# Optimization experiments

Measured on AMD Instinct MI355X. Metric: run time of the kernel, lower is better.

## Reference

```python
import math
import jax, jax.numpy as jnp
import numpy as np


def setup_inputs() -> dict:
    key = jax.random.key(0)
    ks = jax.random.split(key, 11)
    B, L, D = 16, 2048, 1024
    s = 0.02  # weight init scale
    return {
        "queries": jax.random.normal(ks[0], (B, L, D), jnp.float32),
        "keys": jax.random.normal(ks[1], (B, L, D), jnp.float32),
        "values": jax.random.normal(ks[2], (B, L, D), jnp.float32),
        "Wq": jax.random.normal(ks[3], (D, D), jnp.float32) * s,
        "bq": jax.random.normal(ks[4], (D,), jnp.float32) * s,
        "Wk": jax.random.normal(ks[5], (D, D), jnp.float32) * s,
        "bk": jax.random.normal(ks[6], (D,), jnp.float32) * s,
        "Wv": jax.random.normal(ks[7], (D, D), jnp.float32) * s,
        "bv": jax.random.normal(ks[8], (D,), jnp.float32) * s,
        "Wo": jax.random.normal(ks[9], (D, D), jnp.float32) * s,
        "bo": jax.random.normal(ks[10], (D,), jnp.float32) * s,
        "n_heads": 8,
    }


def reference(queries, keys, values, Wq, bq, Wk, bk, Wv, bv, Wo, bo, n_heads):
    B, L, D = queries.shape
    H = n_heads
    E = D // H
    # projections -> (B, H, E, L)
    q = (queries @ Wq.T + bq).reshape(B, L, H, E).transpose(0, 2, 3, 1)
    k = (keys @ Wk.T + bk).reshape(B, L, H, E).transpose(0, 2, 3, 1)
    v = (values @ Wv.T + bv).reshape(B, L, H, E).transpose(0, 2, 3, 1)

    # period-based dependency discovery via FFT cross-correlation
    q_fft = jnp.fft.rfft(q, axis=-1)
    k_fft = jnp.fft.rfft(k, axis=-1)
    corr = jnp.fft.irfft(q_fft * jnp.conj(k_fft), n=L, axis=-1)  # (B,H,E,L)

    # time-delay aggregation (training variant: batch-shared top-k delays)
    top_k = int(1 * math.log(L))  # factor = 1
    mean_value = corr.mean(axis=(1, 2))  # (B, L)
    _, index = jax.lax.top_k(mean_value.mean(axis=0), top_k)  # (top_k,)
    weights = mean_value[:, index]  # (B, top_k)
    tmp_corr = jax.nn.softmax(weights, axis=-1)  # (B, top_k)

    pos = jnp.arange(L)
    agg = jnp.zeros_like(v)
    for i in range(top_k):  # small fixed loop (top_k = 7)
        rolled = jnp.take(v, (pos + index[i]) % L, axis=-1)  # roll(v, -index[i])
        agg = agg + rolled * tmp_corr[:, i][:, None, None, None]

    out = agg.transpose(0, 3, 1, 2).reshape(B, L, D)  # (B,L,H,E) -> (B,L,D)
    return out @ Wo.T + bo
```

## Files before the change

### kernel.cpp

```cpp
#include <hip/hip_runtime.h>

typedef __attribute__((ext_vector_type(8))) short bf16x8;
typedef __attribute__((ext_vector_type(4))) short s16x4;
typedef __attribute__((ext_vector_type(4))) float f32x4;
typedef unsigned short ushort_t;

__device__ __forceinline__ float bf2f(unsigned short u) {
    union { unsigned int u; float f; } x; x.u = ((unsigned int)u) << 16; return x.f;
}
__device__ __forceinline__ unsigned short f2bf(float f) {
    union { float f; unsigned int u; } x; x.f = f;
    unsigned int u = x.u;
    unsigned int r = (u + 0x7fffu + ((u >> 16) & 1u)) >> 16;
    return (unsigned short)r;
}

#define GLDS16(gp, lp)                                                        \
    __builtin_amdgcn_global_load_lds(                                         \
        (const __attribute__((address_space(1))) void*)(gp),                  \
        (__attribute__((address_space(3))) void*)(lp), 16, 0, 0)

template<int OUT_MODE>
__device__ __forceinline__
void gemm_body(const unsigned short* __restrict__ A, const unsigned short* __restrict__ Bw,
               const float* __restrict__ bias, void* __restrict__ out_,
               int bid, int nb, unsigned short* sAp, unsigned short* sBp) {
    const int tid  = threadIdx.x;
    const int lane = tid & 63;
    const int w    = tid >> 6;
    const int wr   = w >> 2, wc = w & 3;
    const int fr   = lane & 15, g4 = lane >> 4;

    const int qq  = nb >> 3;
    const int swz = qq ? (bid & 7) * qq + (bid >> 3) : bid;
    const int  col0 = (swz & 3) * 256;
    const long row0 = (long)(swz >> 2) * 256;

    const int srow = tid >> 3;
    const int sj   = (tid & 7) ^ (srow & 7);
    const unsigned short* gA = A  + (size_t)(row0 + srow) * 1024 + sj * 8;
    const unsigned short* gB = Bw + (size_t)(col0 + srow) * 1024 + sj * 8;
    const int ldst = w * 1024;

    auto stage = [&](int buf, int t) {
        const unsigned short* a = gA + t * 64;
        const unsigned short* b = gB + t * 64;
        char* dA = (char*)(sAp + buf * 16384);
        char* dB = (char*)(sBp + buf * 16384);
#pragma unroll
        for (int r = 0; r < 4; ++r)
            GLDS16(a + r * 65536, (__attribute__((address_space(3))) char*)(dA + r * 8192 + ldst));
#pragma unroll
        for (int r = 0; r < 4; ++r)
            GLDS16(b + r * 65536, (__attribute__((address_space(3))) char*)(dB + r * 8192 + ldst));
    };

    f32x4 acc[8][4];
#pragma unroll
    for (int m = 0; m < 8; ++m)
#pragma unroll
        for (int n = 0; n < 4; ++n) acc[m][n] = (f32x4){0.f, 0.f, 0.f, 0.f};

    stage(0, 0);
    stage(1, 1);

    const int mskK = (fr & 7) << 4;

    for (int t = 0; t < 16; ++t) {
        if (t < 15) asm volatile("s_waitcnt vmcnt(8)" ::: "memory");
        else        asm volatile("s_waitcnt vmcnt(0)" ::: "memory");
        asm volatile("s_barrier" ::: "memory");
        __builtin_amdgcn_sched_barrier(0);

        const char* la = (const char*)(sAp + (t & 1) * 16384);
        const char* lb = (const char*)(sBp + (t & 1) * 16384);

        bf16x8 bF[2][4];
#pragma unroll
        for (int c = 0; c < 2; ++c)
#pragma unroll
            for (int n = 0; n < 4; ++n) {
                const int row = wc * 64 + n * 16 + fr;
                bF[c][n] = *(const bf16x8*)(lb + row * 128 + ((c * 64 + g4 * 16) ^ mskK));
            }
#pragma unroll
        for (int mh = 0; mh < 2; ++mh) {
            bf16x8 aF[2][4];
#pragma unroll
            for (int c = 0; c < 2; ++c)
#pragma unroll
                for (int m = 0; m < 4; ++m) {
                    const int row = wr * 128 + mh * 64 + m * 16 + fr;
                    aF[c][m] = *(const bf16x8*)(la + row * 128 + ((c * 64 + g4 * 16) ^ mskK));
                }
            __builtin_amdgcn_s_setprio(1);
#pragma unroll
            for (int c = 0; c < 2; ++c)
#pragma unroll
                for (int n = 0; n < 4; ++n)
#pragma unroll
                    for (int m = 0; m < 4; ++m)
                        acc[mh * 4 + m][n] =
                            __builtin_amdgcn_mfma_f32_16x16x32_bf16(aF[c][m], bF[c][n], acc[mh * 4 + m][n], 0, 0, 0);
            __builtin_amdgcn_s_setprio(0);
        }

        __builtin_amdgcn_sched_barrier(0);
        asm volatile("s_barrier" ::: "memory");
        if (t + 2 < 16) stage(t & 1, t + 2);
    }

    const int cr = g4 * 4;
    const int cc = fr;
    if constexpr (OUT_MODE == 2) {
        const int b  = (int)(row0 >> 11);
        const int tb = ((int)row0 & 2047) + wr * 128 + cr;
#pragma unroll
        for (int m = 0; m < 8; ++m) {
#pragma unroll
            for (int n = 0; n < 4; ++n) {
                int col = col0 + wc * 64 + n * 16 + cc;
                float bv = bias[col];
                s16x4 o;
#pragma unroll
                for (int j = 0; j < 4; ++j) o[j] = (short)f2bf(acc[m][n][j] + bv);
                *(s16x4*)&((unsigned short*)out_)[((size_t)b * 1024 + col) * 2048 + tb + m * 16] = o;
            }
        }
    } else {
#pragma unroll
        for (int m = 0; m < 8; ++m) {
            long row = row0 + wr * 128 + m * 16 + cr;
#pragma unroll
            for (int n = 0; n < 4; ++n) {
                int col = col0 + wc * 64 + n * 16 + cc;
                float bv = bias[col];
#pragma unroll
                for (int j = 0; j < 4; ++j) {
                    float v = acc[m][n][j] + bv;
                    if constexpr (OUT_MODE == 1) ((float*)out_)[(row + j) * 1024 + col] = v;
                    else ((unsigned short*)out_)[(row + j) * 1024 + col] = f2bf(v);
                }
            }
        }
    }
}

template<int OUT_MODE>
__global__ __launch_bounds__(512, 2)
void gemm256(const unsigned short* __restrict__ A, const unsigned short* __restrict__ Bw,
             const float* __restrict__ bias, void* __restrict__ out_) {
    __shared__ __align__(16) unsigned short sA[2][16384];
    __shared__ __align__(16) unsigned short sB[2][16384];
    gemm_body<OUT_MODE>(A, Bw, bias, out_, blockIdx.x, gridDim.x, &sA[0][0], &sB[0][0]);
}

__global__ __launch_bounds__(512, 2)
void gemm_pair(const unsigned short* __restrict__ A0, const unsigned short* __restrict__ B0,
               const float* __restrict__ bias0, void* __restrict__ o0,
               const unsigned short* __restrict__ A1, const unsigned short* __restrict__ B1,
               const float* __restrict__ bias1, void* __restrict__ o1) {
    __shared__ __align__(16) unsigned short sA[2][16384];
    __shared__ __align__(16) unsigned short sB[2][16384];
    if (blockIdx.x < 16)
        gemm_body<0>(A0, B0, bias0, o0, blockIdx.x, 16, &sA[0][0], &sB[0][0]);
    else
        gemm_body<0>(A1, B1, bias1, o1, blockIdx.x - 16, 16, &sA[0][0], &sB[0][0]);
}

__global__ __launch_bounds__(256)
void cast_f2b(const float* __restrict__ src, unsigned short* __restrict__ dst) {
    const size_t i = ((size_t)blockIdx.x * 256 + threadIdx.x) * 8;
    f32x4 v0 = *(const f32x4*)(src + i);
    f32x4 v1 = *(const f32x4*)(src + i + 4);
    bf16x8 o;
#pragma unroll
    for (int j = 0; j < 4; ++j) o[j] = (short)f2bf(v0[j]);
#pragma unroll
    for (int j = 0; j < 4; ++j) o[4 + j] = (short)f2bf(v1[j]);
    *(bf16x8*)(dst + i) = o;
}

__global__ __launch_bounds__(256)
void prep_all(const float* __restrict__ Wq, const float* __restrict__ Wk,
              const float* __restrict__ Wv, const float* __restrict__ Wo,
              const float* __restrict__ bv, const float* __restrict__ bo,
              unsigned short* __restrict__ wo, unsigned short* __restrict__ wvT,
              unsigned short* __restrict__ wqT, unsigned short* __restrict__ wkT,
              float* __restrict__ G, float* __restrict__ zb, float* __restrict__ b2) {
    __shared__ float tsm[64][65];
    const int bx  = blockIdx.x;
    const int tid = threadIdx.x;

    if (bx < 768) {
        const float* src = (bx < 256) ? Wv : (bx < 512) ? Wq : Wk;
        unsigned short* dst = (bx < 256) ? wvT : (bx < 512) ? wqT : wkT;
        const int t  = bx & 255;
        const int b0 = (t & 15) * 64;
        const int by = (t >> 4) * 64;
        const int tx = tid & 63, ty = tid >> 6;
        for (int r = ty; r < 64; r += 4)
            tsm[r][tx] = src[(size_t)(by + r) * 1024 + b0 + tx];
        __syncthreads();
        for (int r = ty; r < 64; r += 4)
            dst[(size_t)(b0 + r) * 1024 + by + tx] = f2bf(tsm[tx][r]);
    } else if (bx < 1024) {
        const int base = (bx - 768) * 4096 + tid * 4;
#pragma unroll
        for (int r = 0; r < 4; ++r) {
            const int i = base + r * 1024;
            f32x4 v = *(const f32x4*)(Wo + i);
            s16x4 o;
#pragma unroll
            for (int j = 0; j < 4; ++j) o[j] = (short)f2bf(v[j]);
            *(s16x4*)(wo + i) = o;
        }
    } else if (bx < 1033) {
        const int base = (bx - 1024) * 4096;
#pragma unroll
        for (int r = 0; r < 16; ++r) {
            const int i = base + r * 256 + tid;
            if (i < 32800) G[i] = 0.0f;
        }
    } else if (bx == 1033) {
        *(f32x4*)(zb + tid * 4) = (f32x4){0.f, 0.f, 0.f, 0.f};
    } else {
        const int n = (bx - 1034) * 4 + (tid >> 6);
        const int lane = tid & 63;
        float s = 0.f;
        for (int k = lane; k < 1024; k += 64) s += Wo[(size_t)n * 1024 + k] * bv[k];
#pragma unroll
        for (int off = 32; off > 0; off >>= 1) s += __shfl_xor(s, off, 64);
        if (lane == 0) b2[n] = s + bo[n];
    }
}

__device__ __forceinline__ void dft8(float* xr, float* xi) {
    const float c8 = 0.70710678118654752440f;
    float es0r = xr[0] + xr[4], es0i = xi[0] + xi[4];
    float es1r = xr[0] - xr[4], es1i = xi[0] - xi[4];
    float es2r = xr[2] + xr[6], es2i = xi[2] + xi[6];
    float es3r = xr[2] - xr[6], es3i = xi[2] - xi[6];
    float E0r = es0r + es2r, E0i = es0i + es2i;
    float E2r = es0r - es2r, E2i = es0i - es2i;
    float E1r = es1r + es3i, E1i = es1i - es3r;
    float E3r = es1r - es3i, E3i = es1i + es3r;
    float os0r = xr[1] + xr[5], os0i = xi[1] + xi[5];
    float os1r = xr[1] - xr[5], os1i = xi[1] - xi[5];
    float os2r = xr[3] + xr[7], os2i = xi[3] + xi[7];
    float os3r = xr[3] - xr[7], os3i = xi[3] - xi[7];
    float O0r = os0r + os2r, O0i = os0i + os2i;
    float O2r = os0r - os2r, O2i = os0i - os2i;
    float O1r = os1r + os3i, O1i = os1i - os3r;
    float O3r = os1r - os3i, O3i = os1i + os3r;
    float p1 = c8 * (O1r + O1i), q1 = c8 * (O1i - O1r);
    float p3 = c8 * (O3r + O3i), q3 = c8 * (O3i - O3r);
    xr[0] = E0r + O0r; xi[0] = E0i + O0i;
    xr[4] = E0r - O0r; xi[4] = E0i - O0i;
    xr[1] = E1r + p1;  xi[1] = E1i + q1;
    xr[5] = E1r - p1;  xi[5] = E1i - q1;
    xr[2] = E2r + O2i; xi[2] = E2i - O2r;
    xr[6] = E2r - O2i; xi[6] = E2i + O2r;
    xr[3] = E3r + q3;  xi[3] = E3i - p3;
    xr[7] = E3r - q3;  xi[7] = E3i + p3;
}

__device__ __forceinline__ int ps(int p) { return p ^ (((p >> 5) & 7) << 2); }

#define TWIDDLE2(wr_, wi_)                                                    \
    {                                                                         \
        float cr_ = (wr_), ci_ = (wi_);                                       \
        _Pragma("unroll")                                                     \
        for (int k = 1; k < 8; ++k) {                                         \
            float t0 = ar[k] * cr_ - ai[k] * ci_;                             \
            float t1 = ar[k] * ci_ + ai[k] * cr_;                             \
            ar[k] = t0; ai[k] = t1;                                           \
            float t2 = br[k] * cr_ - bi[k] * ci_;                             \
            float t3 = br[k] * ci_ + bi[k] * cr_;                             \
            br[k] = t2; bi[k] = t3;                                           \
            if (k < 7) {                                                      \
                float nr = cr_ * (wr_) - ci_ * (wi_);                         \
                float ni = cr_ * (wi_) + ci_ * (wr_);                         \
                cr_ = nr; ci_ = ni;                                           \
            }                                                                 \
        }                                                                     \
    }

__global__ __launch_bounds__(256)
void fft_corr(const float* __restrict__ qf, const unsigned short* __restrict__ kt,
              float* __restrict__ G) {
    __shared__ float2 za[2048];
    __shared__ float2 zb[2048];
    const int tid = threadIdx.x;
    const int bid = blockIdx.x;
    const int swzb = (bid & 7) * 256 + (bid >> 3);
    const int b = swzb >> 7;
    const int chunk = swzb & 127;

    const float N2PI = -6.28318530717958647692f;
    float w1r, w1i, w2r, w2i, w3r, w3i;
    {
        float s, c;
        __sincosf(N2PI * (float)tid * (1.0f / 2048.0f), &s, &c); w1r = c; w1i = s;
        __sincosf(N2PI * (float)(tid & 31) * (1.0f / 256.0f), &s, &c); w2r = c; w2i = s;
        __sincosf(N2PI * (float)(tid & 3) * (1.0f / 32.0f),  &s, &c); w3r = c; w3i = s;
    }

    f32x4 qreg0[8], qreg1[8];
    {
        const float* qb0 = qf + (size_t)b * 2048 * 1024 + chunk * 8;
#pragma unroll
        for (int k = 0; k < 8; ++k) {
            const float* p = qb0 + (size_t)(tid + 256 * k) * 1024;
            qreg0[k] = *(const f32x4*)p;
            qreg1[k] = *(const f32x4*)(p + 4);
        }
    }

    float aR0 = 0.f, aI0 = 0.f, aR1 = 0.f, aI1 = 0.f;
    float aR2 = 0.f, aI2 = 0.f, aR3 = 0.f, aI3 = 0.f, aR4 = 0.f;

    const int beta = tid >> 5, s2 = tid & 31;
    const int gam  = tid >> 2, u3 = tid & 3;

    for (int it = 0; it < 4; ++it) {
        const int d0 = chunk * 8 + it * 2;
        const unsigned short* k0 = kt + ((size_t)b * 1024 + d0) * 2048;
        const unsigned short* k1 = k0 + 2048;

        float ar[8], ai[8], br[8], bi[8];
#pragma unroll
        for (int k = 0; k < 8; ++k) {
            const int t = tid + 256 * k;
            f32x4 v = (it & 2) ? qreg1[k] : qreg0[k];
            float qa = (it & 1) ? v[2] : v[0];
            float qb = (it & 1) ? v[3] : v[1];
            ar[k] = qa; br[k] = qb;
            ai[k] = bf2f(k0[t]); bi[k] = bf2f(k1[t]);
        }
        dft8(ar, ai); dft8(br, bi);
        TWIDDLE2(w1r, w1i)
#pragma unroll
        for (int k = 0; k < 8; ++k) {
            const int p = ps(256 * k + tid);
            za[p] = make_float2(ar[k], ai[k]);
            zb[p] = make_float2(br[k], bi[k]);
        }
        __syncthreads();

#pragma unroll
        for (int k = 0; k < 8; ++k) {
            const int p = ps(256 * beta + 32 * k + s2);
            float2 va = za[p]; ar[k] = va.x; ai[k] = va.y;
            float2 vb = zb[p]; br[k] = vb.x; bi[k] = vb.y;
        }
        dft8(ar, ai); dft8(br, bi);
        TWIDDLE2(w2r, w2i)
#pragma unroll
        for (int k = 0; k < 8; ++k) {
            const int p = ps(256 * beta + 32 * k + s2);
            za[p] = make_float2(ar[k], ai[k]);
            zb[p] = make_float2(br[k], bi[k]);
        }
        __syncthreads();

#pragma unroll
        for (int k = 0; k < 8; ++k) {
            const int p = ps(32 * gam + 4 * k + u3);
            float2 va = za[p]; ar[k] = va.x; ai[k] = va.y;
            float2 vb = zb[p]; br[k] = vb.x; bi[k] = vb.y;
        }
        dft8(ar, ai); dft8(br, bi);
        TWIDDLE2(w3r, w3i)
#pragma unroll
        for (int k = 0; k < 8; ++k) {
            const int p = ps(32 * gam + 4 * k + u3);
            za[p] = make_float2(ar[k], ai[k]);
            zb[p] = make_float2(br[k], bi[k]);
        }
        __syncthreads();

#pragma unroll
        for (int k = 0; k < 8; ++k) {
            const int p = ps(8 * tid + k);
            float2 va = za[p]; ar[k] = va.x; ai[k] = va.y;
            float2 vb = zb[p]; br[k] = vb.x; bi[k] = vb.y;
        }
        __syncthreads();

#pragma unroll
        for (int blk = 0; blk < 2; ++blk) {
            const int o = 4 * blk;
            {
                float s0r = ar[o] + ar[o + 2], s0i = ai[o] + ai[o + 2];
                float s1r = ar[o] - ar[o + 2], s1i = ai[o] - ai[o + 2];
                float s2r = ar[o + 1] + ar[o + 3], s2i = ai[o + 1] + ai[o + 3];
                float s3r = ar[o + 1] - ar[o + 3], s3i = ai[o + 1] - ai[o + 3];
                ar[o + 0] = s0r + s2r; ai[o + 0] = s0i + s2i;
                ar[o + 2] = s0r - s2r; ai[o + 2] = s0i - s2i;
                ar[o + 1] = s1r + s3i; ai[o + 1] = s1i - s3r;
                ar[o + 3] = s1r - s3i; ai[o + 3] = s1i + s3r;
            }
            {
                float s0r = br[o] + br[o + 2], s0i = bi[o] + bi[o + 2];
                float s1r = br[o] - br[o + 2], s1i = bi[o] - bi[o + 2];
                float s2r = br[o + 1] + br[o + 3], s2i = bi[o + 1] + bi[o + 3];
                float s3r = br[o + 1] - br[o + 3], s3i = bi[o + 1] - bi[o + 3];
                br[o + 0] = s0r + s2r; bi[o + 0] = s0i + s2i;
                br[o + 2] = s0r - s2r; bi[o + 2] = s0i - s2i;
                br[o + 1] = s1r + s3i; bi[o + 1] = s1i - s3r;
                br[o + 3] = s1r - s3i; bi[o + 3] = s1i + s3r;
            }
        }
        {
            const int k1d = tid >> 5;
            const int k2d = (tid >> 2) & 7;
            const int fb = k1d + 8 * k2d;
#pragma unroll
            for (int blk = 0; blk < 2; ++blk) {
                const int k3d = (2 * (tid & 3) + blk) & 7;
#pragma unroll
                for (int k4 = 0; k4 < 4; ++k4) {
                    const int f = fb + 64 * k3d + 512 * k4;
                    const int pf = ps(f);
                    za[pf] = make_float2(ar[4 * blk + k4], ai[4 * blk + k4]);
                    zb[pf] = make_float2(br[4 * blk + k4], bi[4 * blk + k4]);
                }
            }
        }
        __syncthreads();

#pragma unroll
        for (int k = 0; k < 4; ++k) {
            const int f = tid + 256 * k;
            const int f2 = (2048 - f) & 2047;
            const int pf = ps(f), pf2 = ps(f2);
            float2 Za = za[pf], Ya = za[pf2];
            float Qr = 0.5f * (Za.x + Ya.x), Qi = 0.5f * (Za.y - Ya.y);
            float Kr = 0.5f * (Za.y + Ya.y), Ki = -0.5f * (Za.x - Ya.x);
            float dR = Qr * Kr + Qi * Ki;
            float dI = Qi * Kr - Qr * Ki;
            float2 Zb = zb[pf], Yb = zb[pf2];
            Qr = 0.5f * (Zb.x + Yb.x); Qi = 0.5f * (Zb.y - Yb.y);
            Kr = 0.5f * (Zb.y + Yb.y); Ki = -0.5f * (Zb.x - Yb.x);
            dR += Qr * Kr + Qi * Ki;
            dI += Qi * Kr - Qr * Ki;
            if      (k == 0) { aR0 += dR; aI0 += dI; }
            else if (k == 1) { aR1 += dR; aI1 += dI; }
            else if (k == 2) { aR2 += dR; aI2 += dI; }
            else             { aR3 += dR; aI3 += dI; }
        }
        if (tid == 0) {
            const int pf = ps(1024);
            aR4 += za[pf].x * za[pf].y + zb[pf].x * zb[pf].y;
        }
        __syncthreads();
    }

    atomicAdd(&G[((size_t)b * 1025 + tid +   0) * 2 + 0], aR0);
    atomicAdd(&G[((size_t)b * 1025 + tid +   0) * 2 + 1], aI0);
    atomicAdd(&G[((size_t)b * 1025 + tid + 256) * 2 + 0], aR1);
    atomicAdd(&G[((size_t)b * 1025 + tid + 256) * 2 + 1], aI1);
    atomicAdd(&G[((size_t)b * 1025 + tid + 512) * 2 + 0], aR2);
    atomicAdd(&G[((size_t)b * 1025 + tid + 512) * 2 + 1], aI2);
    atomicAdd(&G[((size_t)b * 1025 + tid + 768) * 2 + 0], aR3);
    atomicAdd(&G[((size_t)b * 1025 + tid + 768) * 2 + 1], aI3);
    if (tid == 0)
        atomicAdd(&G[((size_t)b * 1025 + 1024) * 2 + 0], aR4);
}

__device__ __forceinline__ void fft2048(float* zr, float* zi,
                                        const float* twr, const float* twi, int tid) {
    for (int t = tid; t < 2048; t += 256) {
        int j = __brev((unsigned)t) >> 21;
        if (j > t) {
            float a = zr[t]; zr[t] = zr[j]; zr[j] = a;
            float c = zi[t]; zi[t] = zi[j]; zi[j] = c;
        }
    }
    __syncthreads();
    for (int s = 0; s < 11; ++s) {
        const int m = 1 << s;
        for (int i = tid; i < 1024; i += 256) {
            const int pos = i & (m - 1);
            const int i1  = ((i >> s) << (s + 1)) + pos;
            const int i2  = i1 + m;
            const int tw  = pos << (10 - s);
            float wr = twr[tw], wi = twi[tw];
            float xr = zr[i2], xi = zi[i2];
            float tr = wr * xr - wi * xi;
            float ti = wr * xi + wi * xr;
            float ur = zr[i1], ui = zi[i1];
            zr[i2] = ur - tr; zi[i2] = ui - ti;
            zr[i1] = ur + tr; zi[i1] = ui + ti;
        }
        __syncthreads();
    }
}

__device__ __forceinline__ void init_twiddle(float* twr, float* twi, int tid) {
    for (int j = tid; j < 1024; j += 256) {
        float ang = -6.28318530717958647692f * (float)j * (1.0f / 2048.0f);
        twr[j] = cosf(ang);
        twi[j] = sinf(ang);
    }
}

__global__ __launch_bounds__(256)
void irfft_mean(const float* __restrict__ G, float* __restrict__ mv) {
    __shared__ float zr[2048], zi[2048];
    __shared__ float twr[1024], twi[1024];
    const int tid = threadIdx.x;
    const int b = blockIdx.x;
    init_twiddle(twr, twi, tid);
    for (int f = tid; f < 2048; f += 256) {
        int g = (f <= 1024) ? f : 2048 - f;
        float gr = G[((size_t)b * 1025 + g) * 2 + 0];
        float gi = G[((size_t)b * 1025 + g) * 2 + 1];
        zr[f] = gr;
        zi[f] = (f <= 1024) ? -gi : gi;
    }
    __syncthreads();
    fft2048(zr, zi, twr, twi, tid);
    const float sc = 1.0f / (2048.0f * 1024.0f);
    for (int t = tid; t < 2048; t += 256) mv[b * 2048 + t] = zr[t] * sc;
}

__global__ __launch_bounds__(256)
void topk_softmax(const float* __restrict__ mv, int* __restrict__ idx_out,
                  float* __restrict__ w_out) {
    __shared__ float cm[2048];
    __shared__ float wv4[4];
    __shared__ int   wi4[4];
    __shared__ int   sel[7];
    const int tid  = threadIdx.x;
    const int lane = tid & 63;
    const int wvid = tid >> 6;

    for (int t = tid; t < 2048; t += 256) {
        float s = 0.f;
        for (int b = 0; b < 16; ++b) s += mv[b * 2048 + t];
        cm[t] = s * (1.0f / 16.0f);
    }
    __syncthreads();

    for (int it = 0; it < 7; ++it) {
        float best = -3.4e38f; int bi = 1 << 30;
#pragma unroll
        for (int q = 0; q < 8; ++q) {
            const int t = tid + q * 256;
            float v = cm[t];
            if (v > best || (v == best && t < bi)) { best = v; bi = t; }
        }
#pragma unroll
        for (int off = 32; off > 0; off >>= 1) {
            float ov = __shfl_xor(best, off, 64);
            int   oi = __shfl_xor(bi,   off, 64);
            if (ov > best || (ov == best && oi < bi)) { best = ov; bi = oi; }
        }
        if (lane == 0) { wv4[wvid] = best; wi4[wvid] = bi; }
        __syncthreads();
        if (tid == 0) {
            float bb = wv4[0]; int bj = wi4[0];
#pragma unroll
            for (int u = 1; u < 4; ++u)
                if (wv4[u] > bb || (wv4[u] == bb && wi4[u] < bj)) { bb = wv4[u]; bj = wi4[u]; }
            sel[it] = bj;
            idx_out[it] = bj;
            cm[bj] = -3.4e38f;
        }
        __syncthreads();
    }

    if (tid < 16) {
        const int b = tid;
        float wv[7]; float mx = -3.4e38f;
#pragma unroll
        for (int i = 0; i < 7; ++i) { wv[i] = mv[b * 2048 + sel[i]]; mx = fmaxf(mx, wv[i]); }
        float s = 0.f;
#pragma unroll
        for (int i = 0; i < 7; ++i) { wv[i] = expf(wv[i] - mx); s += wv[i]; }
        float inv = 1.0f / s;
#pragma unroll
        for (int i = 0; i < 7; ++i) w_out[b * 7 + i] = wv[i] * inv;
    }
}

__global__ __launch_bounds__(256)
void agg_kernel(const float* __restrict__ vsrc, const int* __restrict__ idx,
                const float* __restrict__ w, unsigned short* __restrict__ agg) {
    const int b  = blockIdx.y;
    const int t  = blockIdx.x * 2 + (threadIdx.x >> 7);
    const int d8 = (threadIdx.x & 127) * 8;
    float av[8] = {0.f, 0.f, 0.f, 0.f, 0.f, 0.f, 0.f, 0.f};
#pragma unroll
    for (int i = 0; i < 7; ++i) {
        const int srow = (t + idx[i]) & 2047;
        const float wi = w[b * 7 + i];
        const float* src = vsrc + ((size_t)b * 2048 + srow) * 1024 + d8;
        f32x4 v0 = *(const f32x4*)src;
        f32x4 v1 = *(const f32x4*)(src + 4);
#pragma unroll
        for (int j = 0; j < 4; ++j) av[j] += wi * v0[j];
#pragma unroll
        for (int j = 0; j < 4; ++j) av[4 + j] += wi * v1[j];
    }
    bf16x8 o;
#pragma unroll
    for (int j = 0; j < 8; ++j) o[j] = (short)f2bf(av[j]);
    *(bf16x8*)&agg[((size_t)b * 2048 + t) * 1024 + d8] = o;
}

extern "C" void kernel_launch(void* const* d_in, const int* in_sizes, int n_in,
                              void* d_out, int out_size, void* d_ws, size_t ws_size,
                              hipStream_t stream) {
    const float* queries = (const float*)d_in[0];
    const float* keys    = (const float*)d_in[1];
    const float* values  = (const float*)d_in[2];
    const float* Wq = (const float*)d_in[3];
    const float* Wk = (const float*)d_in[5];
    const float* Wv = (const float*)d_in[7];  const float* bv = (const float*)d_in[8];
    const float* Wo = (const float*)d_in[9];  const float* bo = (const float*)d_in[10];
    float* out = (float*)d_out;

    char* ws = (char*)d_ws;
    constexpr size_t SZP = (size_t)32768 * 1024 * 2;
    unsigned short* agg = (unsigned short*)(ws);
    unsigned short* kt  = (unsigned short*)(ws + SZP);
    unsigned short* ab  = (unsigned short*)(ws + 3 * SZP);
    unsigned short* wo  = ab;
    unsigned short* wvT = ab + 1048576;
    unsigned short* wqT = ab + 2097152;
    unsigned short* wkT = ab + 3145728;
    unsigned short* W2  = (unsigned short*)(ws + 4 * SZP);
    unsigned short* M   = W2 + 1048576;
    char* tail = ws + 4 * SZP + 4194304;
    float* zb1024 = (float*)(tail);
    float* b2     = (float*)(tail + 4096);
    float* G      = (float*)(tail + 8192);
    float* mv     = (float*)(tail + 8192 + 131328);
    int*   idx    = (int*)  (tail + 8192 + 131328 + 131072);
    float* wsm    = (float*)(tail + 8192 + 131328 + 131072 + 64);

    prep_all<<<1290, 256, 0, stream>>>(Wq, Wk, Wv, Wo, bv, bo,
                                       wo, wvT, wqT, wkT, G, zb1024, b2);
    gemm_pair<<<32, 512, 0, stream>>>(wo, wvT, zb1024, W2,
                                      wqT, wkT, zb1024, M);
    cast_f2b<<<16384, 256, 0, stream>>>(keys, ab);
    gemm256<2><<<512, 512, 0, stream>>>(ab, M, zb1024, kt);

    fft_corr<<<2048, 256, 0, stream>>>(queries, kt, G);
    irfft_mean<<<16, 256, 0, stream>>>(G, mv);
    topk_softmax<<<1, 256, 0, stream>>>(mv, idx, wsm);
    agg_kernel<<<dim3(1024, 16), 256, 0, stream>>>(values, idx, wsm, agg);
    gemm256<1><<<512, 512, 0, stream>>>(agg, W2, b2, out);
}
```

Baseline: 536.8 us.

## Pre-transpose queries to bf16 time-major layout and pad FFT shared memory

A new prep kernel transposes queries into a bf16 (B, D, L) buffer, fused with the existing key cast. The FFT correlation kernel can then read queries with coalesced bf16 loads instead of strided fp32 row loads. The FFT kernel also replaces its XOR-swizzled LDS indexing with padding, stores the final-stage data as separate real and imaginary arrays, and drops the block-index swizzle. The cost is an extra full pass over queries (fp32 read plus bf16 write), and queries are now rounded to bf16 before the correlation.

```diff
diff --git a/kernel.cpp b/kernel.cpp
--- a/kernel.cpp
+++ b/kernel.cpp
@@ -3,7 +3,6 @@
 typedef __attribute__((ext_vector_type(8))) short bf16x8;
 typedef __attribute__((ext_vector_type(4))) short s16x4;
 typedef __attribute__((ext_vector_type(4))) float f32x4;
-typedef unsigned short ushort_t;
 
 __device__ __forceinline__ float bf2f(unsigned short u) {
     union { unsigned int u; float f; } x; x.u = ((unsigned int)u) << 16; return x.f;
@@ -169,16 +168,35 @@
 }
 
 __global__ __launch_bounds__(256)
-void cast_f2b(const float* __restrict__ src, unsigned short* __restrict__ dst) {
-    const size_t i = ((size_t)blockIdx.x * 256 + threadIdx.x) * 8;
-    f32x4 v0 = *(const f32x4*)(src + i);
-    f32x4 v1 = *(const f32x4*)(src + i + 4);
-    bf16x8 o;
-#pragma unroll
-    for (int j = 0; j < 4; ++j) o[j] = (short)f2bf(v0[j]);
-#pragma unroll
-    for (int j = 0; j < 4; ++j) o[4 + j] = (short)f2bf(v1[j]);
-    *(bf16x8*)(dst + i) = o;
+void prep_inputs(const float* __restrict__ queries, const float* __restrict__ keys,
+                 unsigned short* __restrict__ qt, unsigned short* __restrict__ ab) {
+    __shared__ float tsm[64][65];
+    const int bx  = blockIdx.x;
+    const int tid = threadIdx.x;
+    if (bx < 8192) {
+        const int b   = bx >> 9;
+        const int rem = bx & 511;
+        const int t0  = (rem & 31) * 64;
+        const int d0  = (rem >> 5) * 64;
+        const int tx = tid & 63, ty = tid >> 6;
+        const float* s = queries + ((size_t)b * 2048 + t0) * 1024 + d0;
+        for (int r = ty; r < 64; r += 4)
+            tsm[r][tx] = s[(size_t)r * 1024 + tx];
+        __syncthreads();
+        unsigned short* d = qt + ((size_t)b * 1024 + d0) * 2048 + t0;
+        for (int r = ty; r < 64; r += 4)
+            d[(size_t)r * 2048 + tx] = f2bf(tsm[tx][r]);
+    } else {
+        const size_t i = ((size_t)(bx - 8192) * 256 + tid) * 8;
+        f32x4 v0 = *(const f32x4*)(keys + i);
+        f32x4 v1 = *(const f32x4*)(keys + i + 4);
+        bf16x8 o;
+#pragma unroll
+        for (int j = 0; j < 4; ++j) o[j] = (short)f2bf(v0[j]);
+#pragma unroll
+        for (int j = 0; j < 4; ++j) o[4 + j] = (short)f2bf(v1[j]);
+        *(bf16x8*)(ab + i) = o;
+    }
 }
 
 __global__ __launch_bounds__(256)
@@ -265,7 +283,7 @@
     xr[7] = E3r - q3;  xi[7] = E3i + p3;
 }
 
-__device__ __forceinline__ int ps(int p) { return p ^ (((p >> 5) & 7) << 2); }
+__device__ __forceinline__ int padc(int p) { return p + (p >> 5); }
 
 #define TWIDDLE2(wr_, wi_)                                                    \
     {                                                                         \
@@ -287,15 +305,15 @@
     }
 
 __global__ __launch_bounds__(256)
-void fft_corr(const float* __restrict__ qf, const unsigned short* __restrict__ kt,
+void fft_corr(const unsigned short* __restrict__ qt, const unsigned short* __restrict__ kt,
               float* __restrict__ G) {
-    __shared__ float2 za[2048];
-    __shared__ float2 zb[2048];
+    __shared__ float2 za[2112];
+    __shared__ float2 zb[2112];
+    float* zfr0 = (float*)za; float* zfi0 = zfr0 + 2112;
+    float* zfr1 = (float*)zb; float* zfi1 = zfr1 + 2112;
     const int tid = threadIdx.x;
-    const int bid = blockIdx.x;
-    const int swzb = (bid & 7) * 256 + (bid >> 3);
-    const int b = swzb >> 7;
-    const int chunk = swzb & 127;
+    const int b = blockIdx.x >> 7;
+    const int chunk = blockIdx.x & 127;
 
     const float N2PI = -6.28318530717958647692f;
     float w1r, w1i, w2r, w2i, w3r, w3i;
@@ -306,17 +324,6 @@
         __sincosf(N2PI * (float)(tid & 3) * (1.0f / 32.0f),  &s, &c); w3r = c; w3i = s;
     }
 
-    f32x4 qreg0[8], qreg1[8];
-    {
-        const float* qb0 = qf + (size_t)b * 2048 * 1024 + chunk * 8;
-#pragma unroll
-        for (int k = 0; k < 8; ++k) {
-            const float* p = qb0 + (size_t)(tid + 256 * k) * 1024;
-            qreg0[k] = *(const f32x4*)p;
-            qreg1[k] = *(const f32x4*)(p + 4);
-        }
-    }
-
     float aR0 = 0.f, aI0 = 0.f, aR1 = 0.f, aI1 = 0.f;
     float aR2 = 0.f, aI2 = 0.f, aR3 = 0.f, aI3 = 0.f, aR4 = 0.f;
 
@@ -325,24 +332,22 @@
 
     for (int it = 0; it < 4; ++it) {
         const int d0 = chunk * 8 + it * 2;
+        const unsigned short* q0 = qt + ((size_t)b * 1024 + d0) * 2048;
         const unsigned short* k0 = kt + ((size_t)b * 1024 + d0) * 2048;
+        const unsigned short* q1 = q0 + 2048;
         const unsigned short* k1 = k0 + 2048;
 
         float ar[8], ai[8], br[8], bi[8];
 #pragma unroll
         for (int k = 0; k < 8; ++k) {
-            const int t = tid + 256 * k;
-            f32x4 v = (it & 2) ? qreg1[k] : qreg0[k];
-            float qa = (it & 1) ? v[2] : v[0];
-            float qb = (it & 1) ? v[3] : v[1];
-            ar[k] = qa; br[k] = qb;
-            ai[k] = bf2f(k0[t]); bi[k] = bf2f(k1[t]);
+            ar[k] = bf2f(q0[tid + 256 * k]); ai[k] = bf2f(k0[tid + 256 * k]);
+            br[k] = bf2f(q1[tid + 256 * k]); bi[k] = bf2f(k1[tid + 256 * k]);
         }
         dft8(ar, ai); dft8(br, bi);
         TWIDDLE2(w1r, w1i)
 #pragma unroll
         for (int k = 0; k < 8; ++k) {
-            const int p = ps(256 * k + tid);
+            const int p = padc(256 * k + tid);
             za[p] = make_float2(ar[k], ai[k]);
             zb[p] = make_float2(br[k], bi[k]);
         }
@@ -350,7 +355,7 @@
 
 #pragma unroll
         for (int k = 0; k < 8; ++k) {
-            const int p = ps(256 * beta + 32 * k + s2);
+            const int p = padc(256 * beta + 32 * k + s2);
             float2 va = za[p]; ar[k] = va.x; ai[k] = va.y;
             float2 vb = zb[p]; br[k] = vb.x; bi[k] = vb.y;
         }
@@ -358,7 +363,7 @@
         TWIDDLE2(w2r, w2i)
 #pragma unroll
         for (int k = 0; k < 8; ++k) {
-            const int p = ps(256 * beta + 32 * k + s2);
+            const int p = padc(256 * beta + 32 * k + s2);
             za[p] = make_float2(ar[k], ai[k]);
             zb[p] = make_float2(br[k], bi[k]);
         }
@@ -366,7 +371,7 @@
 
 #pragma unroll
         for (int k = 0; k < 8; ++k) {
-            const int p = ps(32 * gam + 4 * k + u3);
+            const int p = padc(32 * gam + 4 * k + u3);
             float2 va = za[p]; ar[k] = va.x; ai[k] = va.y;
             float2 vb = zb[p]; br[k] = vb.x; bi[k] = vb.y;
         }
@@ -374,7 +379,7 @@
         TWIDDLE2(w3r, w3i)
 #pragma unroll
         for (int k = 0; k < 8; ++k) {
-            const int p = ps(32 * gam + 4 * k + u3);
+            const int p = padc(32 * gam + 4 * k + u3);
             za[p] = make_float2(ar[k], ai[k]);
             zb[p] = make_float2(br[k], bi[k]);
         }
@@ -382,7 +387,7 @@
 
 #pragma unroll
         for (int k = 0; k < 8; ++k) {
-            const int p = ps(8 * tid + k);
+            const int p = padc(8 * tid + k);
             float2 va = za[p]; ar[k] = va.x; ai[k] = va.y;
             float2 vb = zb[p]; br[k] = vb.x; bi[k] = vb.y;
         }
@@ -422,9 +427,9 @@
 #pragma unroll
                 for (int k4 = 0; k4 < 4; ++k4) {
                     const int f = fb + 64 * k3d + 512 * k4;
-                    const int pf = ps(f);
-                    za[pf] = make_float2(ar[4 * blk + k4], ai[4 * blk + k4]);
-                    zb[pf] = make_float2(br[4 * blk + k4], bi[4 * blk + k4]);
+                    const int pf = padc(f);
+                    zfr0[pf] = ar[4 * blk + k4]; zfi0[pf] = ai[4 * blk + k4];
+                    zfr1[pf] = br[4 * blk + k4]; zfi1[pf] = bi[4 * blk + k4];
                 }
             }
         }
@@ -434,15 +439,17 @@
         for (int k = 0; k < 4; ++k) {
             const int f = tid + 256 * k;
             const int f2 = (2048 - f) & 2047;
-            const int pf = ps(f), pf2 = ps(f2);
-            float2 Za = za[pf], Ya = za[pf2];
-            float Qr = 0.5f * (Za.x + Ya.x), Qi = 0.5f * (Za.y - Ya.y);
-            float Kr = 0.5f * (Za.y + Ya.y), Ki = -0.5f * (Za.x - Ya.x);
+            const int pf = padc(f), pf2 = padc(f2);
+            float Zr = zfr0[pf],  Zi = zfi0[pf];
+            float Yr = zfr0[pf2], Yi = -zfi0[pf2];
+            float Qr = 0.5f * (Zr + Yr), Qi = 0.5f * (Zi + Yi);
+            float Kr = 0.5f * (Zi - Yi), Ki = -0.5f * (Zr - Yr);
             float dR = Qr * Kr + Qi * Ki;
             float dI = Qi * Kr - Qr * Ki;
-            float2 Zb = zb[pf], Yb = zb[pf2];
-            Qr = 0.5f * (Zb.x + Yb.x); Qi = 0.5f * (Zb.y - Yb.y);
-            Kr = 0.5f * (Zb.y + Yb.y); Ki = -0.5f * (Zb.x - Yb.x);
+            Zr = zfr1[pf];  Zi = zfi1[pf];
+            Yr = zfr1[pf2]; Yi = -zfi1[pf2];
+            Qr = 0.5f * (Zr + Yr); Qi = 0.5f * (Zi + Yi);
+            Kr = 0.5f * (Zi - Yi); Ki = -0.5f * (Zr - Yr);
             dR += Qr * Kr + Qi * Ki;
             dI += Qi * Kr - Qr * Ki;
             if      (k == 0) { aR0 += dR; aI0 += dI; }
@@ -451,8 +458,8 @@
             else             { aR3 += dR; aI3 += dI; }
         }
         if (tid == 0) {
-            const int pf = ps(1024);
-            aR4 += za[pf].x * za[pf].y + zb[pf].x * zb[pf].y;
+            const int pf = padc(1024);
+            aR4 += zfr0[pf] * zfi0[pf] + zfr1[pf] * zfi1[pf];
         }
         __syncthreads();
     }
@@ -627,6 +634,7 @@
     constexpr size_t SZP = (size_t)32768 * 1024 * 2;
     unsigned short* agg = (unsigned short*)(ws);
     unsigned short* kt  = (unsigned short*)(ws + SZP);
+    unsigned short* qt  = (unsigned short*)(ws + 2 * SZP);
     unsigned short* ab  = (unsigned short*)(ws + 3 * SZP);
     unsigned short* wo  = ab;
     unsigned short* wvT = ab + 1048576;
@@ -646,10 +654,10 @@
                                        wo, wvT, wqT, wkT, G, zb1024, b2);
     gemm_pair<<<32, 512, 0, stream>>>(wo, wvT, zb1024, W2,
                                       wqT, wkT, zb1024, M);
-    cast_f2b<<<16384, 256, 0, stream>>>(keys, ab);
+    prep_inputs<<<24576, 256, 0, stream>>>(queries, keys, qt, ab);
     gemm256<2><<<512, 512, 0, stream>>>(ab, M, zb1024, kt);
 
-    fft_corr<<<2048, 256, 0, stream>>>(queries, kt, G);
+    fft_corr<<<2048, 256, 0, stream>>>(qt, kt, G);
     irfft_mean<<<16, 256, 0, stream>>>(G, mv);
     topk_softmax<<<1, 256, 0, stream>>>(mv, idx, wsm);
     agg_kernel<<<dim3(1024, 16), 256, 0, stream>>>(values, idx, wsm, agg);
```

Measured after the change: 509.4 us. 1.05x faster.
